# Performance work log

Measured on AMD Instinct MI355X. Metric: run time of the kernel, lower is better.

The kernel has to match this reference:

```python
import jax, jax.numpy as jnp
import numpy as np

N_USERS = 19968
N_ITEMS = 6144
EMBED = 64
V_DIM = 4096
T_DIM = 384
KNN_K = 10
LAMBDA = 0.9          # lambda_coeff
N_LAYERS = 1          # item-graph propagation layers
N_UI_LAYERS = 2       # len(weight_size)
NNZ = 600000


def build_sim(x):
    # cosine similarity: row-normalize then x @ x.T  -> [N, N]
    xn = x / jnp.linalg.norm(x, axis=-1, keepdims=True)
    return xn @ xn.T


def knn_graph(adj, k):
    # torch.topk + scatter_: keep top-k values per row, zeros elsewhere
    vals, idx = jax.lax.top_k(adj, k)                      # [N, k]
    rows = jnp.arange(adj.shape[0])[:, None]
    return jnp.zeros_like(adj).at[rows, idx].set(vals)


def norm_laplacian(adj):
    # D^{-1/2} A D^{-1/2} with inf -> 0
    d = jnp.sum(adj, axis=-1) ** -0.5
    d = jnp.where(jnp.isinf(d), 0.0, d)
    return adj * d[:, None] * d[None, :]


def setup_inputs() -> dict:
    key = jax.random.key(0)
    ks = jax.random.split(key, 10)
    user_emb = jax.random.normal(ks[0], (N_USERS, EMBED), jnp.float32) * 0.1
    item_emb = jax.random.normal(ks[1], (N_ITEMS, EMBED), jnp.float32) * 0.1
    image_feat = jax.random.normal(ks[2], (N_ITEMS, V_DIM), jnp.float32)
    text_feat = jax.random.normal(ks[3], (N_ITEMS, T_DIM), jnp.float32)
    image_trs_w = jax.random.normal(ks[4], (V_DIM, EMBED), jnp.float32) * 0.02
    image_trs_b = jnp.zeros((EMBED,), jnp.float32)
    text_trs_w = jax.random.normal(ks[5], (T_DIM, EMBED), jnp.float32) * 0.05
    text_trs_b = jnp.zeros((EMBED,), jnp.float32)
    modal_weight = jnp.array([0.5, 0.5], jnp.float32)
    # frozen buffers: knn laplacians built from the raw multimodal features
    image_orig_adj = norm_laplacian(knn_graph(build_sim(image_feat), KNN_K))
    text_orig_adj = norm_laplacian(knn_graph(build_sim(text_feat), KNN_K))
    n_nodes = N_USERS + N_ITEMS
    rows = jax.random.randint(ks[6], (NNZ,), 0, n_nodes, dtype=jnp.int32)
    cols = jax.random.randint(ks[7], (NNZ,), 0, n_nodes, dtype=jnp.int32)
    adj_indices = jnp.stack([rows, cols], axis=0)           # [2, NNZ] COO
    adj_values = jax.random.uniform(ks[8], (NNZ,), jnp.float32) * 0.01
    return {
        "user_emb": user_emb, "item_emb": item_emb,
        "image_feat": image_feat, "text_feat": text_feat,
        "image_trs_w": image_trs_w, "image_trs_b": image_trs_b,
        "text_trs_w": text_trs_w, "text_trs_b": text_trs_b,
        "modal_weight": modal_weight,
        "image_orig_adj": image_orig_adj, "text_orig_adj": text_orig_adj,
        "adj_indices": adj_indices, "adj_values": adj_values,
        "knn_k": KNN_K,
    }


def reference(user_emb, item_emb, image_feat, text_feat,
              image_trs_w, image_trs_b, text_trs_w, text_trs_b,
              modal_weight, image_orig_adj, text_orig_adj,
              adj_indices, adj_values, knn_k):
    # modality projections
    image_feats = image_feat @ image_trs_w + image_trs_b   # [N_items, 64]
    text_feats = text_feat @ text_trs_w + text_trs_b       # [N_items, 64]
    w = jax.nn.softmax(modal_weight)
    # build_item_graph=True branch
    image_adj = knn_graph(build_sim(image_feats), knn_k)
    text_adj = knn_graph(build_sim(text_feats), knn_k)
    learned_adj = norm_laplacian(w[0] * image_adj + w[1] * text_adj)
    original_adj = w[0] * image_orig_adj + w[1] * text_orig_adj
    item_adj = (1.0 - LAMBDA) * learned_adj + LAMBDA * original_adj
    # item-graph propagation
    h = item_emb
    for _ in range(N_LAYERS):
        h = item_adj @ h
    # lightgcn user-item propagation via sparse COO matmul
    ego = jnp.concatenate([user_emb, item_emb], axis=0)    # [n_nodes, 64]
    n_nodes = ego.shape[0]
    src, dst = adj_indices[0], adj_indices[1]
    all_emb = [ego]
    for _ in range(N_UI_LAYERS):
        ego = jax.ops.segment_sum(adj_values[:, None] * ego[dst], src,
                                  num_segments=n_nodes)
        all_emb.append(ego)
    all_emb = jnp.mean(jnp.stack(all_emb, axis=1), axis=1)
    u_g = all_emb[:N_USERS]
    h_norm = h / jnp.maximum(jnp.linalg.norm(h, axis=1, keepdims=True), 1e-12)
    i_g = all_emb[N_USERS:] + h_norm
    return u_g, i_g
```

## Files before the change

### kernel.cpp

```cpp
#include <hip/hip_runtime.h>
#include <hip/hip_bf16.h>

#define NU 19968
#define NI 6144
#define NNODE (NU + NI)
#define EMB 64
#define VD 4096
#define TD 384
#define NNZE 600000
#define LAMB 0.9f
#define NCH 8
#define CPC (NI / NCH)

typedef __attribute__((ext_vector_type(8))) short bf16x8;
typedef __attribute__((ext_vector_type(4))) float f32x4;
#define MFMA16(a, b, c) __builtin_amdgcn_mfma_f32_16x16x32_bf16(a, b, c, 0, 0, 0)


__device__ __forceinline__ void topk_insert(float (&cv)[10], int (&ci)[10], float v, int j) {
    if (v <= cv[9]) return;
#pragma unroll
    for (int s = 0; s < 10; ++s) {
        if (v > cv[s]) {
            float tv = cv[s]; cv[s] = v; v = tv;
            int tj = ci[s]; ci[s] = j; j = tj;
        }
    }
}

__device__ __forceinline__ float2 softmax2(const float* mw) {
    float e0 = expf(mw[0]), e1 = expf(mw[1]);
    float inv = 1.0f / (e0 + e1);
    return make_float2(e0 * inv, e1 * inv);
}

__device__ __forceinline__ unsigned short f2bf(float f) {
    unsigned int u = __float_as_uint(f);
    unsigned int r = (u + 0x7FFFu + ((u >> 16) & 1u)) >> 16;
    return (unsigned short)r;
}
__device__ __forceinline__ float bf2f(unsigned short h) { return __uint_as_float(((unsigned int)h) << 16); }


__global__ __launch_bounds__(256) void gemm_tr(const float* __restrict__ A, const float* __restrict__ W,
                                               float* __restrict__ C, int M, int K, int kps) {
    __shared__ float At[64][64];
    __shared__ float Wt[64][64];
    const int t = threadIdx.x;
    const int m0 = blockIdx.x * 64;
    const int k0 = blockIdx.y * kps;
    const int tm = t & 15, tn = t >> 4;
    float acc[4][4] = {};
    for (int kt = k0; kt < k0 + kps; kt += 64) {
        __syncthreads();
        for (int i = t; i < 1024; i += 256) {
            int m = i >> 4, k4 = (i & 15) << 2;
            float4 v = *(const float4*)(A + (size_t)(m0 + m) * K + kt + k4);
            At[k4 + 0][m] = v.x; At[k4 + 1][m] = v.y; At[k4 + 2][m] = v.z; At[k4 + 3][m] = v.w;
        }
        for (int i = t; i < 1024; i += 256) {
            int kk = i >> 4, n4 = (i & 15) << 2;
            *(float4*)&Wt[kk][n4] = *(const float4*)(W + (size_t)(kt + kk) * 64 + n4);
        }
        __syncthreads();
#pragma unroll
        for (int kk = 0; kk < 64; ++kk) {
            float a[4], b[4];
            *(float4*)a = *(const float4*)&At[kk][tm << 2];
            *(float4*)b = *(const float4*)&Wt[kk][tn << 2];
#pragma unroll
            for (int i = 0; i < 4; ++i)
#pragma unroll
                for (int j = 0; j < 4; ++j) acc[i][j] += a[i] * b[j];
        }
    }
#pragma unroll
    for (int i = 0; i < 4; ++i)
#pragma unroll
        for (int j = 0; j < 4; ++j)
            unsafeAtomicAdd(&C[(size_t)(m0 + (tm << 2) + i) * 64 + (tn << 2) + j], acc[i][j]);
}


__global__ __launch_bounds__(256) void rownorm(const float* __restrict__ C, const float* __restrict__ bias,
                                               unsigned short* __restrict__ xh, unsigned short* __restrict__ xl) {
    int row = blockIdx.x * 4 + (threadIdx.x >> 6);
    int lane = threadIdx.x & 63;
    float v = C[(size_t)row * 64 + lane] + bias[lane];
    float ss = v * v;
#pragma unroll
    for (int o = 32; o; o >>= 1) ss += __shfl_xor(ss, o, 64);
    float xn = v * (1.0f / sqrtf(ss));
    unsigned short h = f2bf(xn);
    float lo = xn - bf2f(h);
    xh[(size_t)row * 64 + lane] = h;
    xl[(size_t)row * 64 + lane] = f2bf(lo);
}


__global__ __launch_bounds__(256) void sims_topk_mfma(const unsigned short* __restrict__ xh_img,
                                                      const unsigned short* __restrict__ xl_img,
                                                      const unsigned short* __restrict__ xh_txt,
                                                      const unsigned short* __restrict__ xl_txt,
                                                      float* __restrict__ tkv, int* __restrict__ tki) {
    const unsigned short* xh = blockIdx.z ? xh_txt : xh_img;
    const unsigned short* xl = blockIdx.z ? xl_txt : xl_img;
    const int r0 = blockIdx.x * 64;
    const int c0 = blockIdx.y * CPC;
    const int t = threadIdx.x;
    const int wave = t >> 6, lane = t & 63;
    const int fr = lane & 15, fq = lane >> 4;

    const size_t abase = (size_t)(r0 + wave * 16 + fr) * 64 + fq * 8;
    bf16x8 ahi0 = *(const bf16x8*)(xh + abase);
    bf16x8 ahi1 = *(const bf16x8*)(xh + abase + 32);
    bf16x8 alo0 = *(const bf16x8*)(xl + abase);
    bf16x8 alo1 = *(const bf16x8*)(xl + abase + 32);

    float cv[4][10]; int ci[4][10];
#pragma unroll
    for (int r = 0; r < 4; ++r)
#pragma unroll
        for (int s = 0; s < 10; ++s) { cv[r][s] = -INFINITY; ci[r][s] = 0; }

    for (int ct = 0; ct < CPC / 64; ++ct) {
        const int cbase = c0 + ct * 64;
#pragma unroll
        for (int cs = 0; cs < 4; ++cs) {
            const int c = cbase + cs * 16 + fr;
            const size_t bbase = (size_t)c * 64 + fq * 8;
            bf16x8 bhi0 = *(const bf16x8*)(xh + bbase);
            bf16x8 bhi1 = *(const bf16x8*)(xh + bbase + 32);
            bf16x8 blo0 = *(const bf16x8*)(xl + bbase);
            bf16x8 blo1 = *(const bf16x8*)(xl + bbase + 32);
            f32x4 a = {0.f, 0.f, 0.f, 0.f};
            a = MFMA16(ahi0, bhi0, a);
            a = MFMA16(ahi1, bhi1, a);
            a = MFMA16(ahi0, blo0, a);
            a = MFMA16(ahi1, blo1, a);
            a = MFMA16(alo0, bhi0, a);
            a = MFMA16(alo1, bhi1, a);
#pragma unroll
            for (int r = 0; r < 4; ++r) topk_insert(cv[r], ci[r], a[r], c);
        }
    }

#pragma unroll
    for (int m = 1; m <= 8; m <<= 1) {
#pragma unroll
        for (int r = 0; r < 4; ++r) {
            float ov[10]; int oi[10];
#pragma unroll
            for (int s = 0; s < 10; ++s) {
                ov[s] = __shfl_xor(cv[r][s], m);
                oi[s] = __shfl_xor(ci[r][s], m);
            }
#pragma unroll
            for (int s = 0; s < 10; ++s) topk_insert(cv[r], ci[r], ov[s], oi[s]);
        }
    }

    if (fr == 0) {
#pragma unroll
        for (int r = 0; r < 4; ++r) {
            int row = r0 + wave * 16 + fq * 4 + r;
            size_t base = ((size_t)(blockIdx.z * NI + row) * NCH + blockIdx.y) * 10;
#pragma unroll
            for (int s = 0; s < 10; ++s) { tkv[base + s] = cv[r][s]; tki[base + s] = ci[r][s]; }
        }
    }
}


__global__ void merge_chunks(const float* __restrict__ tkv, const int* __restrict__ tki,
                             float* __restrict__ fvv, int* __restrict__ fii) {
    int g = blockIdx.x * blockDim.x + threadIdx.x;
    if (g >= 2 * NI) return;
    float cv[10]; int ci[10];
#pragma unroll
    for (int s = 0; s < 10; ++s) { cv[s] = -INFINITY; ci[s] = 0; }
    for (int u = 0; u < NCH * 10; ++u) topk_insert(cv, ci, tkv[(size_t)g * NCH * 10 + u], tki[(size_t)g * NCH * 10 + u]);
#pragma unroll
    for (int s = 0; s < 10; ++s) { fvv[(size_t)g * 10 + s] = cv[s]; fii[(size_t)g * 10 + s] = ci[s]; }
}


__global__ void calc_dinv(const float* __restrict__ fvv, const float* __restrict__ mw, float* __restrict__ dinv) {
    int i = blockIdx.x * blockDim.x + threadIdx.x;
    if (i >= NI) return;
    float2 w = softmax2(mw);
    float s = 0.f;
    for (int u = 0; u < 10; ++u) s += w.x * fvv[(size_t)i * 10 + u];
    for (int u = 0; u < 10; ++u) s += w.y * fvv[(size_t)(NI + i) * 10 + u];
    dinv[i] = (s > 0.f) ? (1.0f / sqrtf(s)) : 0.f;
}


__global__ __launch_bounds__(256) void compute_h(const float* __restrict__ img_o, const float* __restrict__ txt_o,
                                                 const float* __restrict__ item_emb,
                                                 const float* __restrict__ fvv, const int* __restrict__ fii,
                                                 const float* __restrict__ dinv, const float* __restrict__ mw,
                                                 float* __restrict__ hnorm) {
    const int i = blockIdx.x;
    const int t = threadIdx.x;
    __shared__ int   sj[64];
    __shared__ float sc[64];
    __shared__ int   scnt;
    __shared__ float part[4][64];
    if (t == 0) scnt = 0;
    __syncthreads();
    float2 w = softmax2(mw);
    const float4* ro = (const float4*)(img_o + (size_t)i * NI);
    const float4* to = (const float4*)(txt_o + (size_t)i * NI);
    for (int u = t; u < NI / 4; u += 256) {
        float4 a = ro[u], b = to[u];
        float c[4] = { w.x * a.x + w.y * b.x, w.x * a.y + w.y * b.y,
                       w.x * a.z + w.y * b.z, w.x * a.w + w.y * b.w };
#pragma unroll
        for (int q = 0; q < 4; ++q)
            if (c[q] != 0.f) { int p = atomicAdd(&scnt, 1); sj[p] = u * 4 + q; sc[p] = LAMB * c[q]; }
    }
    if (t < 20) {
        int m = t / 10, s = t % 10;
        float v = fvv[((size_t)m * NI + i) * 10 + s];
        int   j = fii[((size_t)m * NI + i) * 10 + s];
        float wm = m ? w.y : w.x;
        float c = (1.0f - LAMB) * wm * v * dinv[i] * dinv[j];
        int p = atomicAdd(&scnt, 1); sj[p] = j; sc[p] = c;
    }
    __syncthreads();
    const int cnt = scnt;
    const int dim = t & 63, q = t >> 6;
    float acc = 0.f;
    for (int e = q; e < cnt; e += 4) acc += sc[e] * item_emb[(size_t)sj[e] * 64 + dim];
    part[q][dim] = acc;
    __syncthreads();
    if (t < 64) {
        float h = part[0][t] + part[1][t] + part[2][t] + part[3][t];
        float ss = h * h;
#pragma unroll
        for (int o = 32; o; o >>= 1) ss += __shfl_xor(ss, o, 64);
        float scale = 1.0f / fmaxf(sqrtf(ss), 1e-12f);
        hnorm[(size_t)i * 64 + t] = h * scale;
    }
}


__global__ void hist_k(const int* __restrict__ aidx, int* __restrict__ cnt) {
    int e = blockIdx.x * 256 + threadIdx.x;
    if (e < NNZE) atomicAdd(&cnt[aidx[e]], 1);
}

__global__ void scan_partial(const int* __restrict__ cnt, int* __restrict__ rp, int* __restrict__ partials) {
    __shared__ int sm[256];
    int t = threadIdx.x;
    int i = blockIdx.x * 256 + t;
    int v = cnt[i];
    sm[t] = v;
    __syncthreads();
    for (int o = 1; o < 256; o <<= 1) {
        int x = (t >= o) ? sm[t - o] : 0;
        __syncthreads();
        sm[t] += x;
        __syncthreads();
    }
    rp[i] = sm[t] - v;
    if (t == 255) partials[blockIdx.x] = sm[255];
}

__global__ void scan_totals(int* __restrict__ partials, int* __restrict__ rp) {
    if (threadIdx.x == 0) {
        int s = 0;
        for (int b = 0; b < NNODE / 256; ++b) { int v = partials[b]; partials[b] = s; s += v; }
        rp[NNODE] = s;
    }
}

__global__ void add_off(int* __restrict__ rp, const int* __restrict__ partials, int* __restrict__ fill) {
    int i = blockIdx.x * 256 + threadIdx.x;
    int v = rp[i] + partials[blockIdx.x];
    rp[i] = v;
    fill[i] = v;
}

__global__ void scatter_k(const int* __restrict__ aidx, const float* __restrict__ avals,
                          int* __restrict__ fill, int* __restrict__ cdst, float* __restrict__ cval) {
    int e = blockIdx.x * 256 + threadIdx.x;
    if (e >= NNZE) return;
    int src = aidx[e];
    int p = atomicAdd(&fill[src], 1);
    cdst[p] = aidx[NNZE + e];
    cval[p] = avals[e];
}


__global__ __launch_bounds__(256) void ui_gather(const float* __restrict__ uin, const float* __restrict__ iin,
                                                 const float* __restrict__ full_in,
                                                 const int* __restrict__ rp, const int* __restrict__ cdst,
                                                 const float* __restrict__ cval, float* __restrict__ out) {
    int row = blockIdx.x * 4 + (threadIdx.x >> 6);
    int lane = threadIdx.x & 63;
    int s = rp[row], e = rp[row + 1];
    float acc = 0.f;
    int p = s;
    for (; p + 2 <= e; p += 2) {
        int d0 = cdst[p], d1 = cdst[p + 1];
        float v0 = cval[p], v1 = cval[p + 1];
        const float* r0 = full_in ? full_in + (size_t)d0 * 64
                                  : (d0 < NU ? uin + (size_t)d0 * 64 : iin + (size_t)(d0 - NU) * 64);
        const float* r1 = full_in ? full_in + (size_t)d1 * 64
                                  : (d1 < NU ? uin + (size_t)d1 * 64 : iin + (size_t)(d1 - NU) * 64);
        acc += v0 * r0[lane];
        acc += v1 * r1[lane];
    }
    if (p < e) {
        int d0 = cdst[p]; float v0 = cval[p];
        const float* r0 = full_in ? full_in + (size_t)d0 * 64
                                  : (d0 < NU ? uin + (size_t)d0 * 64 : iin + (size_t)(d0 - NU) * 64);
        acc += v0 * r0[lane];
    }
    out[(size_t)row * 64 + lane] = acc;
}


__global__ __launch_bounds__(256) void final_out(const float* __restrict__ ue, const float* __restrict__ ie,
                                                 const float* __restrict__ e1, const float* __restrict__ e2,
                                                 const float* __restrict__ hnorm, float* __restrict__ out) {
    int g = blockIdx.x * 256 + threadIdx.x;
    if (g >= NNODE * 16) return;
    int n = g >> 4;
    float4 a = (n < NU) ? ((const float4*)ue)[g] : ((const float4*)ie)[g - NU * 16];
    float4 b = ((const float4*)e1)[g];
    float4 c = ((const float4*)e2)[g];
    const float third = 1.0f / 3.0f;
    float4 r;
    r.x = (a.x + b.x + c.x) * third;
    r.y = (a.y + b.y + c.y) * third;
    r.z = (a.z + b.z + c.z) * third;
    r.w = (a.w + b.w + c.w) * third;
    if (n >= NU) {
        float4 h = ((const float4*)hnorm)[g - NU * 16];
        r.x += h.x; r.y += h.y; r.z += h.z; r.w += h.w;
    }
    ((float4*)out)[g] = r;
}


extern "C" void kernel_launch(void* const* d_in, const int* in_sizes, int n_in,
                              void* d_out, int out_size, void* d_ws, size_t ws_size,
                              hipStream_t stream) {
    const float* user_emb   = (const float*)d_in[0];
    const float* item_emb   = (const float*)d_in[1];
    const float* image_feat = (const float*)d_in[2];
    const float* text_feat  = (const float*)d_in[3];
    const float* img_w      = (const float*)d_in[4];
    const float* img_b      = (const float*)d_in[5];
    const float* txt_w      = (const float*)d_in[6];
    const float* txt_b      = (const float*)d_in[7];
    const float* mw         = (const float*)d_in[8];
    const float* img_orig   = (const float*)d_in[9];
    const float* txt_orig   = (const float*)d_in[10];
    const int*   aidx       = (const int*)d_in[11];
    const float* avals      = (const float*)d_in[12];

    float* C_img = (float*)d_ws;
    float* C_txt = C_img + (size_t)NI * EMB;
    unsigned short* xh_img = (unsigned short*)(C_txt + (size_t)NI * EMB);
    unsigned short* xl_img = xh_img + (size_t)NI * EMB;
    unsigned short* xh_txt = xl_img + (size_t)NI * EMB;
    unsigned short* xl_txt = xh_txt + (size_t)NI * EMB;
    float* tk_val  = (float*)(xl_txt + (size_t)NI * EMB);
    int*   tk_idx  = (int*)(tk_val + (size_t)2 * NI * NCH * 10);
    float* fin_val = (float*)(tk_idx + (size_t)2 * NI * NCH * 10);
    int*   fin_idx = (int*)(fin_val + 2 * NI * 10);
    float* dinv    = (float*)(fin_idx + 2 * NI * 10);
    float* hnorm   = dinv + NI;
    float* ego1    = hnorm + (size_t)NI * EMB;
    float* ego2    = ego1 + (size_t)NNODE * EMB;
    int* cnt      = (int*)(ego2 + (size_t)NNODE * EMB);
    int* row_ptr  = cnt + NNODE;
    int* fill     = row_ptr + NNODE + 1;
    int* partials = fill + NNODE;
    int* csr_dst  = partials + 128;
    float* csr_val = (float*)(csr_dst + NNZE);

    hipMemsetAsync(C_img, 0, (size_t)NI * EMB * 4, stream);
    hipMemsetAsync(C_txt, 0, (size_t)NI * EMB * 4, stream);
    hipMemsetAsync(cnt, 0, (size_t)NNODE * 4, stream);

    hist_k<<<(NNZE + 255) / 256, 256, 0, stream>>>(aidx, cnt);
    scan_partial<<<NNODE / 256, 256, 0, stream>>>(cnt, row_ptr, partials);
    scan_totals<<<1, 64, 0, stream>>>(partials, row_ptr);
    add_off<<<NNODE / 256, 256, 0, stream>>>(row_ptr, partials, fill);
    scatter_k<<<(NNZE + 255) / 256, 256, 0, stream>>>(aidx, avals, fill, csr_dst, csr_val);

    gemm_tr<<<dim3(NI / 64, 8), 256, 0, stream>>>(image_feat, img_w, C_img, NI, VD, VD / 8);
    gemm_tr<<<dim3(NI / 64, 6), 256, 0, stream>>>(text_feat,  txt_w, C_txt, NI, TD, TD / 6);

    rownorm<<<NI / 4, 256, 0, stream>>>(C_img, img_b, xh_img, xl_img);
    rownorm<<<NI / 4, 256, 0, stream>>>(C_txt, txt_b, xh_txt, xl_txt);

    sims_topk_mfma<<<dim3(NI / 64, NCH, 2), 256, 0, stream>>>(xh_img, xl_img, xh_txt, xl_txt, tk_val, tk_idx);

    merge_chunks<<<(2 * NI + 255) / 256, 256, 0, stream>>>(tk_val, tk_idx, fin_val, fin_idx);

    calc_dinv<<<(NI + 255) / 256, 256, 0, stream>>>(fin_val, mw, dinv);

    compute_h<<<NI, 256, 0, stream>>>(img_orig, txt_orig, item_emb, fin_val, fin_idx, dinv, mw, hnorm);

    ui_gather<<<NNODE / 4, 256, 0, stream>>>(user_emb, item_emb, nullptr, row_ptr, csr_dst, csr_val, ego1);
    ui_gather<<<NNODE / 4, 256, 0, stream>>>(user_emb, item_emb, ego1,    row_ptr, csr_dst, csr_val, ego2);

    final_out<<<(NNODE * 16 + 255) / 256, 256, 0, stream>>>(user_emb, item_emb, ego1, ego2, hnorm, (float*)d_out);
}
```

Baseline: 1.058 ms.

## Split similarity top-k into value-only threshold pass and candidate-collect recompute pass

The fused sim+top-k kernel is replaced by two passes. The first keeps only top-10 values with branchless min/max insertion and an early-exit warp merge, which yields a per-row threshold. The second recomputes the similarities and atomically collects the entries at or above that threshold into a small candidate buffer, and a final kernel picks the top-10 with index tie-breaking. This removes index tracking from the hot loop, which cuts register pressure and swap work. The cost is running the MFMA similarity computation twice, and rows with more than 16 tied candidates are truncated.

```diff
diff --git a/kernel.cpp b/kernel.cpp
--- a/kernel.cpp
+++ b/kernel.cpp
@@ -11,17 +11,27 @@
 #define LAMB 0.9f
 #define NCH 8
 #define CPC (NI / NCH)
+#define MAXC 16
 
 typedef __attribute__((ext_vector_type(8))) short bf16x8;
 typedef __attribute__((ext_vector_type(4))) float f32x4;
 #define MFMA16(a, b, c) __builtin_amdgcn_mfma_f32_16x16x32_bf16(a, b, c, 0, 0, 0)
 
 
-__device__ __forceinline__ void topk_insert(float (&cv)[10], int (&ci)[10], float v, int j) {
-    if (v <= cv[9]) return;
+__device__ __forceinline__ void vins(float (&cv)[10], float v) {
 #pragma unroll
     for (int s = 0; s < 10; ++s) {
-        if (v > cv[s]) {
+        float mx = fmaxf(cv[s], v);
+        v = fminf(cv[s], v);
+        cv[s] = mx;
+    }
+}
+
+__device__ __forceinline__ void topk_ins_tie(float (&cv)[10], int (&ci)[10], float v, int j) {
+#pragma unroll
+    for (int s = 0; s < 10; ++s) {
+        bool take = (v > cv[s]) || (v == cv[s] && j < ci[s]);
+        if (take) {
             float tv = cv[s]; cv[s] = v; v = tv;
             int tj = ci[s]; ci[s] = j; j = tj;
         }
@@ -40,6 +50,25 @@
     return (unsigned short)r;
 }
 __device__ __forceinline__ float bf2f(unsigned short h) { return __uint_as_float(((unsigned int)h) << 16); }
+
+__device__ __forceinline__ f32x4 sim_tile(const unsigned short* __restrict__ xh,
+                                          const unsigned short* __restrict__ xl,
+                                          bf16x8 ahi0, bf16x8 ahi1, bf16x8 alo0, bf16x8 alo1,
+                                          int c, int fq) {
+    const size_t bbase = (size_t)c * 64 + fq * 8;
+    bf16x8 bhi0 = *(const bf16x8*)(xh + bbase);
+    bf16x8 bhi1 = *(const bf16x8*)(xh + bbase + 32);
+    bf16x8 blo0 = *(const bf16x8*)(xl + bbase);
+    bf16x8 blo1 = *(const bf16x8*)(xl + bbase + 32);
+    f32x4 a = {0.f, 0.f, 0.f, 0.f};
+    a = MFMA16(ahi0, bhi0, a);
+    a = MFMA16(ahi1, bhi1, a);
+    a = MFMA16(ahi0, blo0, a);
+    a = MFMA16(ahi1, blo1, a);
+    a = MFMA16(alo0, bhi0, a);
+    a = MFMA16(alo1, bhi1, a);
+    return a;
+}
 
 
 __global__ __launch_bounds__(256) void gemm_tr(const float* __restrict__ A, const float* __restrict__ W,
@@ -98,11 +127,11 @@
 }
 
 
-__global__ __launch_bounds__(256) void sims_topk_mfma(const unsigned short* __restrict__ xh_img,
-                                                      const unsigned short* __restrict__ xl_img,
-                                                      const unsigned short* __restrict__ xh_txt,
-                                                      const unsigned short* __restrict__ xl_txt,
-                                                      float* __restrict__ tkv, int* __restrict__ tki) {
+__global__ __launch_bounds__(256) void sims_tauA(const unsigned short* __restrict__ xh_img,
+                                                 const unsigned short* __restrict__ xl_img,
+                                                 const unsigned short* __restrict__ xh_txt,
+                                                 const unsigned short* __restrict__ xl_txt,
+                                                 float* __restrict__ tkv) {
     const unsigned short* xh = blockIdx.z ? xh_txt : xh_img;
     const unsigned short* xl = blockIdx.z ? xl_txt : xl_img;
     const int r0 = blockIdx.x * 64;
@@ -117,31 +146,20 @@
     bf16x8 alo0 = *(const bf16x8*)(xl + abase);
     bf16x8 alo1 = *(const bf16x8*)(xl + abase + 32);
 
-    float cv[4][10]; int ci[4][10];
+    float cv[4][10];
 #pragma unroll
     for (int r = 0; r < 4; ++r)
 #pragma unroll
-        for (int s = 0; s < 10; ++s) { cv[r][s] = -INFINITY; ci[r][s] = 0; }
+        for (int s = 0; s < 10; ++s) cv[r][s] = -INFINITY;
 
     for (int ct = 0; ct < CPC / 64; ++ct) {
         const int cbase = c0 + ct * 64;
 #pragma unroll
         for (int cs = 0; cs < 4; ++cs) {
-            const int c = cbase + cs * 16 + fr;
-            const size_t bbase = (size_t)c * 64 + fq * 8;
-            bf16x8 bhi0 = *(const bf16x8*)(xh + bbase);
-            bf16x8 bhi1 = *(const bf16x8*)(xh + bbase + 32);
-            bf16x8 blo0 = *(const bf16x8*)(xl + bbase);
-            bf16x8 blo1 = *(const bf16x8*)(xl + bbase + 32);
-            f32x4 a = {0.f, 0.f, 0.f, 0.f};
-            a = MFMA16(ahi0, bhi0, a);
-            a = MFMA16(ahi1, bhi1, a);
-            a = MFMA16(ahi0, blo0, a);
-            a = MFMA16(ahi1, blo1, a);
-            a = MFMA16(alo0, bhi0, a);
-            a = MFMA16(alo1, bhi1, a);
-#pragma unroll
-            for (int r = 0; r < 4; ++r) topk_insert(cv[r], ci[r], a[r], c);
+            f32x4 a = sim_tile(xh, xl, ahi0, ahi1, alo0, alo1, cbase + cs * 16 + fr, fq);
+#pragma unroll
+            for (int r = 0; r < 4; ++r)
+                if (a[r] > cv[r][9]) vins(cv[r], a[r]);
         }
     }
 
@@ -149,14 +167,17 @@
     for (int m = 1; m <= 8; m <<= 1) {
 #pragma unroll
         for (int r = 0; r < 4; ++r) {
-            float ov[10]; int oi[10];
+            float ov[10];
+#pragma unroll
+            for (int s = 0; s < 10; ++s) ov[s] = __shfl_xor(cv[r][s], m);
+            bool done = false;
 #pragma unroll
             for (int s = 0; s < 10; ++s) {
-                ov[s] = __shfl_xor(cv[r][s], m);
-                oi[s] = __shfl_xor(ci[r][s], m);
+                if (!done) {
+                    if (__all(ov[s] <= cv[r][9])) done = true;
+                    else if (ov[s] > cv[r][9]) vins(cv[r], ov[s]);
+                }
             }
-#pragma unroll
-            for (int s = 0; s < 10; ++s) topk_insert(cv[r], ci[r], ov[s], oi[s]);
         }
     }
 
@@ -166,20 +187,87 @@
             int row = r0 + wave * 16 + fq * 4 + r;
             size_t base = ((size_t)(blockIdx.z * NI + row) * NCH + blockIdx.y) * 10;
 #pragma unroll
-            for (int s = 0; s < 10; ++s) { tkv[base + s] = cv[r][s]; tki[base + s] = ci[r][s]; }
-        }
-    }
-}
-
-
-__global__ void merge_chunks(const float* __restrict__ tkv, const int* __restrict__ tki,
-                             float* __restrict__ fvv, int* __restrict__ fii) {
+            for (int s = 0; s < 10; ++s) tkv[base + s] = cv[r][s];
+        }
+    }
+}
+
+
+__global__ void tau_merge(const float* __restrict__ tkv, float* __restrict__ tau) {
+    int g = blockIdx.x * blockDim.x + threadIdx.x;
+    if (g >= 2 * NI) return;
+    float cv[10];
+#pragma unroll
+    for (int s = 0; s < 10; ++s) cv[s] = -INFINITY;
+    for (int u = 0; u < NCH * 10; ++u) {
+        float v = tkv[(size_t)g * NCH * 10 + u];
+        if (v > cv[9]) vins(cv, v);
+    }
+    tau[g] = cv[9];
+}
+
+
+__global__ __launch_bounds__(256) void sims_collect(const unsigned short* __restrict__ xh_img,
+                                                    const unsigned short* __restrict__ xl_img,
+                                                    const unsigned short* __restrict__ xh_txt,
+                                                    const unsigned short* __restrict__ xl_txt,
+                                                    const float* __restrict__ tau,
+                                                    int* __restrict__ ccnt,
+                                                    float* __restrict__ cval, int* __restrict__ ccol) {
+    const unsigned short* xh = blockIdx.z ? xh_txt : xh_img;
+    const unsigned short* xl = blockIdx.z ? xl_txt : xl_img;
+    const int r0 = blockIdx.x * 64;
+    const int c0 = blockIdx.y * CPC;
+    const int t = threadIdx.x;
+    const int wave = t >> 6, lane = t & 63;
+    const int fr = lane & 15, fq = lane >> 4;
+
+    const size_t abase = (size_t)(r0 + wave * 16 + fr) * 64 + fq * 8;
+    bf16x8 ahi0 = *(const bf16x8*)(xh + abase);
+    bf16x8 ahi1 = *(const bf16x8*)(xh + abase + 32);
+    bf16x8 alo0 = *(const bf16x8*)(xl + abase);
+    bf16x8 alo1 = *(const bf16x8*)(xl + abase + 32);
+
+    float tv[4];
+    int grow[4];
+#pragma unroll
+    for (int r = 0; r < 4; ++r) {
+        grow[r] = blockIdx.z * NI + r0 + wave * 16 + fq * 4 + r;
+        tv[r] = tau[grow[r]];
+    }
+
+    for (int ct = 0; ct < CPC / 64; ++ct) {
+        const int cbase = c0 + ct * 64;
+#pragma unroll
+        for (int cs = 0; cs < 4; ++cs) {
+            const int c = cbase + cs * 16 + fr;
+            f32x4 a = sim_tile(xh, xl, ahi0, ahi1, alo0, alo1, c, fq);
+#pragma unroll
+            for (int r = 0; r < 4; ++r) {
+                if (a[r] >= tv[r]) {
+                    int p = atomicAdd(&ccnt[grow[r]], 1);
+                    if (p < MAXC) {
+                        cval[(size_t)grow[r] * MAXC + p] = a[r];
+                        ccol[(size_t)grow[r] * MAXC + p] = c;
+                    }
+                }
+            }
+        }
+    }
+}
+
+
+__global__ void topk_cand(const int* __restrict__ ccnt, const float* __restrict__ cval,
+                          const int* __restrict__ ccol,
+                          float* __restrict__ fvv, int* __restrict__ fii) {
     int g = blockIdx.x * blockDim.x + threadIdx.x;
     if (g >= 2 * NI) return;
     float cv[10]; int ci[10];
 #pragma unroll
-    for (int s = 0; s < 10; ++s) { cv[s] = -INFINITY; ci[s] = 0; }
-    for (int u = 0; u < NCH * 10; ++u) topk_insert(cv, ci, tkv[(size_t)g * NCH * 10 + u], tki[(size_t)g * NCH * 10 + u]);
+    for (int s = 0; s < 10; ++s) { cv[s] = -INFINITY; ci[s] = 0x7fffffff; }
+    int n = ccnt[g]; if (n > MAXC) n = MAXC;
+    for (int u = 0; u < n; ++u)
+        topk_ins_tie(cv, ci, cval[(size_t)g * MAXC + u], ccol[(size_t)g * MAXC + u]);
 #pragma unroll
     for (int s = 0; s < 10; ++s) { fvv[(size_t)g * 10 + s] = cv[s]; fii[(size_t)g * 10 + s] = ci[s]; }
 }
@@ -369,9 +457,12 @@
     unsigned short* xl_img = xh_img + (size_t)NI * EMB;
     unsigned short* xh_txt = xl_img + (size_t)NI * EMB;
     unsigned short* xl_txt = xh_txt + (size_t)NI * EMB;
-    float* tk_val  = (float*)(xl_txt + (size_t)NI * EMB);
-    int*   tk_idx  = (int*)(tk_val + (size_t)2 * NI * NCH * 10);
-    float* fin_val = (float*)(tk_idx + (size_t)2 * NI * NCH * 10);
+    float* tkvA    = (float*)(xl_txt + (size_t)NI * EMB);
+    float* tau     = tkvA + (size_t)2 * NI * NCH * 10;
+    int*   ccnt    = (int*)(tau + 2 * NI);
+    float* candv   = (float*)(ccnt + 2 * NI);
+    int*   candc   = (int*)(candv + (size_t)2 * NI * MAXC);
+    float* fin_val = (float*)(candc + (size_t)2 * NI * MAXC);
     int*   fin_idx = (int*)(fin_val + 2 * NI * 10);
     float* dinv    = (float*)(fin_idx + 2 * NI * 10);
     float* hnorm   = dinv + NI;
@@ -387,6 +478,7 @@
     hipMemsetAsync(C_img, 0, (size_t)NI * EMB * 4, stream);
     hipMemsetAsync(C_txt, 0, (size_t)NI * EMB * 4, stream);
     hipMemsetAsync(cnt, 0, (size_t)NNODE * 4, stream);
+    hipMemsetAsync(ccnt, 0, (size_t)2 * NI * 4, stream);
 
     hist_k<<<(NNZE + 255) / 256, 256, 0, stream>>>(aidx, cnt);
     scan_partial<<<NNODE / 256, 256, 0, stream>>>(cnt, row_ptr, partials);
@@ -400,9 +492,11 @@
     rownorm<<<NI / 4, 256, 0, stream>>>(C_img, img_b, xh_img, xl_img);
     rownorm<<<NI / 4, 256, 0, stream>>>(C_txt, txt_b, xh_txt, xl_txt);
 
-    sims_topk_mfma<<<dim3(NI / 64, NCH, 2), 256, 0, stream>>>(xh_img, xl_img, xh_txt, xl_txt, tk_val, tk_idx);
-
-    merge_chunks<<<(2 * NI + 255) / 256, 256, 0, stream>>>(tk_val, tk_idx, fin_val, fin_idx);
+    sims_tauA<<<dim3(NI / 64, NCH, 2), 256, 0, stream>>>(xh_img, xl_img, xh_txt, xl_txt, tkvA);
+    tau_merge<<<(2 * NI + 255) / 256, 256, 0, stream>>>(tkvA, tau);
+    sims_collect<<<dim3(NI / 64, NCH, 2), 256, 0, stream>>>(xh_img, xl_img, xh_txt, xl_txt,
+                                                            tau, ccnt, candv, candc);
+    topk_cand<<<(2 * NI + 255) / 256, 256, 0, stream>>>(ccnt, candv, candc, fin_val, fin_idx);
 
     calc_dinv<<<(NI + 255) / 256, 256, 0, stream>>>(fin_val, mw, dinv);
 
```

New measurement: 1.034 ms. 1.02x faster.
